# Kernel optimization log

Measured on AMD Instinct MI355X. Metric: run time of the kernel, lower is better.

The kernel has to match this reference:

```python
import jax, jax.numpy as jnp
import numpy as np

B, N, F, L, H, C = 128, 512, 128, 64, 128, 10

def setup_inputs() -> dict:
    key = jax.random.key(0)
    ks = jax.random.split(key, 20)
    s = 0.1
    return {
        "g": jax.random.uniform(ks[0], (B, N, N), dtype=jnp.float32) + 1e-3,
        "h": jax.random.normal(ks[1], (B, N, F), dtype=jnp.float32),
        "labels": jax.random.randint(ks[2], (B,), 0, C),
        "eps": jax.random.normal(ks[3], (B, N, 1), dtype=jnp.float32),
        "W_s": jax.random.normal(ks[4], (F, L), dtype=jnp.float32) * s,
        "b_s": jnp.zeros((L,), jnp.float32),
        "W_mu": jax.random.normal(ks[5], (L, 1), dtype=jnp.float32) * s,
        "b_mu": jnp.zeros((1,), jnp.float32),
        "W_lv": jax.random.normal(ks[6], (L, 1), dtype=jnp.float32) * s,
        "b_lv": jnp.zeros((1,), jnp.float32),
        "W_dec": jax.random.normal(ks[7], (1, L), dtype=jnp.float32) * s,
        "b_dec": jnp.zeros((L,), jnp.float32),
        "W1": jax.random.normal(ks[8], (L, H), dtype=jnp.float32) * s,
        "b1": jnp.zeros((H,), jnp.float32),
        "W2": jax.random.normal(ks[9], (H, C), dtype=jnp.float32) * s,
        "b2": jnp.zeros((C,), jnp.float32),
        "beta": jnp.array([50.0], jnp.float32),
    }

def _gcn(gn, x, W, b):
    # GCN layer: propagate then project then ELU activation (dropout = 0)
    return jax.nn.elu(jnp.einsum('bnm,bmf->bnf', gn, x) @ W + b)

def reference(g, h, labels, eps, W_s, b_s, W_mu, b_mu, W_lv, b_lv, W_dec, b_dec, W1, b1, W2, b2, beta):
    # norm_g: degrees = sum over dim 1; broadcast division normalizes COLUMNS
    # (torch g/degrees with degrees of shape [N] divides g[:, j] by degrees[j])
    deg = jnp.sum(g, axis=1)                      # [B, N]
    gn = g / deg[:, None, :]                      # column-normalized adjacency
    h1 = _gcn(gn, h, W_s, b_s)                    # [B, N, L]
    mu = _gcn(gn, h1, W_mu, b_mu)                 # [B, N, 1]
    lv = _gcn(gn, h1, W_lv, b_lv)                 # [B, N, 1]
    z = mu + eps * jnp.exp(0.5 * lv)              # reparameterize (training)
    v = jax.nn.sigmoid(beta[0] * z)               # [B, N, 1]
    d = _gcn(gn, v, W_dec, b_dec)                 # [B, N, L]
    hp = jnp.einsum('bnl,bn->bl', h1, v[..., 0])  # h.T @ v pooling -> [B, L]
    logits = jax.nn.log_softmax(jax.nn.elu(hp @ W1 + b1) @ W2 + b2, axis=1)
    nll = -jnp.mean(logits[jnp.arange(B), labels])
    mus = mu.reshape(-1, 1)
    lvs = lv.reshape(-1, 1)
    M = mus.shape[0]
    kl = (-0.5 / M) * jnp.mean(jnp.sum(1.0 + 2.0 * lvs - mus**2 - jnp.exp(lvs)**2, axis=1))
    mse = jnp.mean((h1 - d) ** 2)
    loss = nll + kl + mse
    acc = jnp.mean((jnp.argmax(logits, axis=1) == labels).astype(jnp.float32))
    return (loss, acc)
```

## Files before the change

### kernel.cpp

```cpp
#include <hip/hip_runtime.h>

#define B_  128
#define N_  512
#define F_  128
#define L_  64
#define H_  128
#define C_  10

typedef short  bf8_t  __attribute__((ext_vector_type(8)));
typedef float  f32x4  __attribute__((ext_vector_type(4)));
typedef unsigned short us8 __attribute__((ext_vector_type(8)));
typedef unsigned short us4 __attribute__((ext_vector_type(4)));

static __device__ __forceinline__ unsigned short f2bf(float x) {
    union { float f; unsigned u; } c; c.f = x;
    unsigned r = (c.u + 0x7fffu + ((c.u >> 16) & 1u)) >> 16;
    return (unsigned short)r;
}
static __device__ __forceinline__ float bf2f(unsigned short s) {
    union { unsigned u; float f; } c; c.u = ((unsigned)s) << 16;
    return c.f;
}
static __device__ __forceinline__ float elu(float x) { return x > 0.f ? x : expm1f(x); }

#define OFF_DEGP   0
#define OFF_DEG    524288
#define OFF_HPP    589824
#define OFF_KLP    655360
#define OFF_MSEP   655872
#define OFF_TMU    656896
#define OFF_TLV    722432
#define OFF_V      787968
#define OFF_W      853504
#define OFF_LP     919040
#define OFF_COR    919168
#define OFF_H1Q    919296
#define OFF_GBF    3016448
#define OFF_UBFT   19793664
#define OFF_WSTBF  21890816

__global__ __launch_bounds__(256) void k1_deg(const float* __restrict__ g,
                                              const float* __restrict__ Ws,
                                              float* __restrict__ deg_part,
                                              unsigned short* __restrict__ gbf,
                                              unsigned short* __restrict__ WsTbf) {
    const int c = blockIdx.x, b = blockIdx.y;
    if (c == 0 && b == 0) {
        for (int i = threadIdx.x; i < F_ * L_; i += 256) {
            int l = i >> 7, f = i & 127;
            WsTbf[i] = f2bf(Ws[f * L_ + l]);
        }
    }
    const int half = threadIdx.x >> 7, lane = threadIdx.x & 127;
    const int j  = lane * 4;
    const int i0 = c * 128 + half * 64;
    const float*    gp = g   + ((size_t)b * N_ + i0) * N_ + j;
    unsigned short* gq = gbf + ((size_t)b * N_ + i0) * N_ + j;
    float4 acc = make_float4(0.f, 0.f, 0.f, 0.f);
    #pragma unroll 8
    for (int r = 0; r < 64; ++r) {
        float4 v = *reinterpret_cast<const float4*>(gp + (size_t)r * N_);
        acc.x += v.x; acc.y += v.y; acc.z += v.z; acc.w += v.w;
        us4 q; q[0] = f2bf(v.x); q[1] = f2bf(v.y); q[2] = f2bf(v.z); q[3] = f2bf(v.w);
        *reinterpret_cast<us4*>(gq + (size_t)r * N_) = q;
    }
    *reinterpret_cast<float4*>(deg_part + (size_t)(b * 8 + c * 2 + half) * N_ + j) = acc;
}

__global__ __launch_bounds__(256) void k2_u(const float* __restrict__ h,
                                            const unsigned short* __restrict__ WsTbf,
                                            const float* __restrict__ deg_part,
                                            float* __restrict__ deg,
                                            unsigned short* __restrict__ ubfT) {
    __shared__ float tile[64 * 65];
    __shared__ float sdeg[64];
    const int b    = blockIdx.y;
    const int m0   = blockIdx.x * 64;
    const int tid  = threadIdx.x;
    const int wave = tid >> 6, lane = tid & 63;
    const int ml = lane & 15, q = lane >> 4;
    const int row0 = wave * 16;

    if (tid < 64) {
        int j = m0 + tid;
        float s = 0.f;
        #pragma unroll
        for (int k = 0; k < 8; ++k) s += deg_part[(size_t)(b * 8 + k) * N_ + j];
        sdeg[tid] = s;
        deg[b * N_ + j] = s;
    }

    const float* A = h + (size_t)(b * N_ + m0 + row0 + ml) * F_ + q * 8;
    const unsigned short* Bb = WsTbf + ml * F_ + q * 8;

    f32x4 acc[4] = {};
    #pragma unroll
    for (int kk = 0; kk < F_; kk += 32) {
        float4 a0 = *reinterpret_cast<const float4*>(A + kk);
        float4 a1 = *reinterpret_cast<const float4*>(A + kk + 4);
        union { unsigned short s[8]; bf8_t v; } av;
        av.s[0] = f2bf(a0.x); av.s[1] = f2bf(a0.y); av.s[2] = f2bf(a0.z); av.s[3] = f2bf(a0.w);
        av.s[4] = f2bf(a1.x); av.s[5] = f2bf(a1.y); av.s[6] = f2bf(a1.z); av.s[7] = f2bf(a1.w);
        #pragma unroll
        for (int i = 0; i < 4; ++i) {
            bf8_t bv = *reinterpret_cast<const bf8_t*>(Bb + i * 16 * F_ + kk);
            acc[i] = __builtin_amdgcn_mfma_f32_16x16x32_bf16(av.v, bv, acc[i], 0, 0, 0);
        }
    }
    __syncthreads();
    #pragma unroll
    for (int i = 0; i < 4; ++i) {
        int col = i * 16 + ml;
        #pragma unroll
        for (int r = 0; r < 4; ++r) {
            int rl = row0 + 4 * q + r;
            tile[rl * 65 + col] = acc[i][r] / sdeg[rl];
        }
    }
    __syncthreads();
    for (int jj = 0; jj < 16; ++jj) {
        int ll = wave + jj * 4;
        ubfT[(size_t)(b * L_ + ll) * N_ + m0 + lane] = f2bf(tile[lane * 65 + ll]);
    }
}

__global__ __launch_bounds__(256) void k3_h1(const unsigned short* __restrict__ gbf,
                                             const unsigned short* __restrict__ ubfT,
                                             const float* __restrict__ b_s,
                                             const float* __restrict__ Wmu,
                                             const float* __restrict__ Wlv,
                                             const float* __restrict__ deg,
                                             unsigned short* __restrict__ h1q,
                                             float* __restrict__ tmu, float* __restrict__ tlv) {
    const int b    = blockIdx.y;
    const int tid  = threadIdx.x;
    const int wave = tid >> 6, lane = tid & 63;
    const int row0 = blockIdx.x * 64 + wave * 16;
    const int ml = lane & 15, q = lane >> 4;

    const unsigned short* A  = gbf  + (size_t)(b * N_ + row0 + ml) * N_ + q * 8;
    const unsigned short* B0 = ubfT + (size_t)(b * L_ + ml) * N_ + q * 8;

    f32x4 acc[4] = {};
    #pragma unroll 2
    for (int k = 0; k < N_; k += 32) {
        bf8_t a = *reinterpret_cast<const bf8_t*>(A + k);
        #pragma unroll
        for (int i = 0; i < 4; ++i) {
            bf8_t bb = *reinterpret_cast<const bf8_t*>(B0 + (size_t)i * 16 * N_ + k);
            acc[i] = __builtin_amdgcn_mfma_f32_16x16x32_bf16(a, bb, acc[i], 0, 0, 0);
        }
    }
    float bsv[4], wm[4], wl[4];
    #pragma unroll
    for (int i = 0; i < 4; ++i) {
        int col = i * 16 + ml;
        bsv[i] = b_s[col]; wm[i] = Wmu[col]; wl[i] = Wlv[col];
    }
    #pragma unroll
    for (int r = 0; r < 4; ++r) {
        int row = row0 + 4 * q + r;
        float pm = 0.f, pl = 0.f;
        #pragma unroll
        for (int i = 0; i < 4; ++i) {
            float hv = elu(acc[i][r] + bsv[i]);
            h1q[(size_t)(b * N_ + row) * L_ + i * 16 + ml] = f2bf(hv);
            pm = fmaf(hv, wm[i], pm);
            pl = fmaf(hv, wl[i], pl);
        }
        #pragma unroll
        for (int o = 1; o < 16; o <<= 1) { pm += __shfl_xor(pm, o); pl += __shfl_xor(pl, o); }
        if (ml == 0) {
            float idg = 1.f / deg[b * N_ + row];
            tmu[b * N_ + row] = pm * idg;
            tlv[b * N_ + row] = pl * idg;
        }
    }
}

__global__ __launch_bounds__(256) void k5_v(const unsigned short* __restrict__ gbf,
                                            const float* __restrict__ tmu, const float* __restrict__ tlv,
                                            const float* __restrict__ eps, const float* __restrict__ deg,
                                            const float* __restrict__ bmu, const float* __restrict__ blv,
                                            const float* __restrict__ beta,
                                            float* __restrict__ v, float* __restrict__ w,
                                            float* __restrict__ kl_part) {
    __shared__ float kls[4];
    const int b = blockIdx.y;
    const int wave = threadIdx.x >> 6, lane = threadIdx.x & 63;
    const int n0 = (blockIdx.x * 4 + wave) * 32;

    const float* tmr = tmu + b * N_ + lane * 8;
    const float* tlr = tlv + b * N_ + lane * 8;
    float tm[8], tl[8];
    *reinterpret_cast<float4*>(tm)     = *reinterpret_cast<const float4*>(tmr);
    *reinterpret_cast<float4*>(tm + 4) = *reinterpret_cast<const float4*>(tmr + 4);
    *reinterpret_cast<float4*>(tl)     = *reinterpret_cast<const float4*>(tlr);
    *reinterpret_cast<float4*>(tl + 4) = *reinterpret_cast<const float4*>(tlr + 4);

    const unsigned short* gbase = gbf + (size_t)(b * N_ + n0) * N_ + lane * 8;
    float myamu = 0.f, myalv = 0.f;
    #pragma unroll 4
    for (int r = 0; r < 32; ++r) {
        us8 gv = *reinterpret_cast<const us8*>(gbase + (size_t)r * N_);
        float amu = 0.f, alv = 0.f;
        #pragma unroll
        for (int j = 0; j < 8; ++j) {
            float gf = bf2f(gv[j]);
            amu = fmaf(gf, tm[j], amu);
            alv = fmaf(gf, tl[j], alv);
        }
        #pragma unroll
        for (int o = 32; o; o >>= 1) { amu += __shfl_xor(amu, o); alv += __shfl_xor(alv, o); }
        if (lane == r) { myamu = amu; myalv = alv; }
    }
    float klv = 0.f;
    if (lane < 32) {
        int n = n0 + lane;
        float mu = elu(myamu + bmu[0]);
        float lv = elu(myalv + blv[0]);
        float z  = mu + eps[b * N_ + n] * expf(0.5f * lv);
        float vv = 1.f / (1.f + expf(-beta[0] * z));
        v[b * N_ + n] = vv;
        w[b * N_ + n] = vv / deg[b * N_ + n];
        float e = expf(lv);
        klv = 1.f + 2.f * lv - mu * mu - e * e;
    }
    #pragma unroll
    for (int o = 32; o; o >>= 1) klv += __shfl_xor(klv, o);
    if (lane == 0) kls[wave] = klv;
    __syncthreads();
    if (threadIdx.x == 0)
        kl_part[blockIdx.y * 4 + blockIdx.x] = kls[0] + kls[1] + kls[2] + kls[3];
}

__global__ __launch_bounds__(256) void k6_dec(const unsigned short* __restrict__ gbf,
                                              const float* __restrict__ w, const float* __restrict__ v,
                                              const unsigned short* __restrict__ h1q,
                                              const float* __restrict__ Wdec, const float* __restrict__ bdec,
                                              float* __restrict__ hp_part, float* __restrict__ mse_part) {
    __shared__ float hps[4 * 64];
    __shared__ float mses[4];
    const int b = blockIdx.y;
    const int n0 = blockIdx.x * 64;
    const int tid = threadIdx.x, wave = tid >> 6, lane = tid & 63;
    const float wd = Wdec[lane], bd = bdec[lane];

    const float* wrow = w + b * N_ + lane * 8;
    float wr[8];
    *reinterpret_cast<float4*>(wr)     = *reinterpret_cast<const float4*>(wrow);
    *reinterpret_cast<float4*>(wr + 4) = *reinterpret_cast<const float4*>(wrow + 4);

    const unsigned short* gbase = gbf + (size_t)(b * N_ + n0 + wave * 16) * N_ + lane * 8;
    float hpl = 0.f, msep = 0.f;
    #pragma unroll 2
    for (int t = 0; t < 16; ++t) {
        int n = n0 + wave * 16 + t;
        us8 gv = *reinterpret_cast<const us8*>(gbase + (size_t)t * N_);
        float p = 0.f;
        #pragma unroll
        for (int j = 0; j < 8; ++j) p = fmaf(bf2f(gv[j]), wr[j], p);
        #pragma unroll
        for (int o = 32; o; o >>= 1) p += __shfl_xor(p, o);
        float dv = elu(p * wd + bd);
        float h1v = bf2f(h1q[(size_t)(b * N_ + n) * L_ + lane]);
        float diff = h1v - dv;
        msep = fmaf(diff, diff, msep);
        hpl  = fmaf(h1v, v[b * N_ + n], hpl);
    }
    hps[wave * 64 + lane] = hpl;
    #pragma unroll
    for (int o = 32; o; o >>= 1) msep += __shfl_xor(msep, o);
    if (lane == 0) mses[wave] = msep;
    __syncthreads();
    if (tid < 64) {
        float s = hps[tid] + hps[64 + tid] + hps[128 + tid] + hps[192 + tid];
        hp_part[(size_t)blockIdx.x * (B_ * 64) + b * 64 + tid] = s;
    }
    if (tid == 0)
        mse_part[blockIdx.y * 8 + blockIdx.x] = mses[0] + mses[1] + mses[2] + mses[3];
}

__global__ __launch_bounds__(128) void k7a_head(const float* __restrict__ hp_part,
                                                const float* __restrict__ W1, const float* __restrict__ b1,
                                                const float* __restrict__ W2, const float* __restrict__ b2,
                                                const int* __restrict__ labels,
                                                float* __restrict__ lp, float* __restrict__ cor) {
    __shared__ float hps[64];
    __shared__ float acts[128];
    __shared__ float lgs[10];
    const int b = blockIdx.x, tid = threadIdx.x;
    if (tid < 64) {
        float s = 0.f;
        #pragma unroll
        for (int x = 0; x < 8; ++x) s += hp_part[(size_t)x * (B_ * 64) + b * 64 + tid];
        hps[tid] = s;
    }
    __syncthreads();
    float s0 = 0, s1 = 0, s2 = 0, s3 = 0;
    for (int l = 0; l < 64; l += 4) {
        s0 += hps[l]     * W1[(l)     * H_ + tid];
        s1 += hps[l + 1] * W1[(l + 1) * H_ + tid];
        s2 += hps[l + 2] * W1[(l + 2) * H_ + tid];
        s3 += hps[l + 3] * W1[(l + 3) * H_ + tid];
    }
    acts[tid] = elu((s0 + s1) + (s2 + s3) + b1[tid]);
    __syncthreads();
    if (tid < C_) {
        float lg = b2[tid];
        for (int hh = 0; hh < H_; ++hh) lg += acts[hh] * W2[hh * C_ + tid];
        lgs[tid] = lg;
    }
    __syncthreads();
    if (tid == 0) {
        float mx = lgs[0]; int am = 0;
        for (int c = 1; c < C_; ++c) if (lgs[c] > mx) { mx = lgs[c]; am = c; }
        float se = 0.f;
        for (int c = 0; c < C_; ++c) se += expf(lgs[c] - mx);
        int lbl = labels[b];
        lp[b]  = lgs[lbl] - mx - logf(se);
        cor[b] = (am == lbl) ? 1.f : 0.f;
    }
}

__global__ __launch_bounds__(128) void k7b_final(const float* __restrict__ lp, const float* __restrict__ cor,
                                                 const float* __restrict__ kl_part, const float* __restrict__ mse_part,
                                                 float* __restrict__ out) {
    __shared__ float r1[128], r2[128], r3[128], r4[128];
    int tid = threadIdx.x;
    r1[tid] = lp[tid]; r2[tid] = cor[tid];
    float k = 0.f, m = 0.f;
    #pragma unroll
    for (int i = 0; i < 4; ++i)  k += kl_part[tid + i * 128];
    #pragma unroll
    for (int i = 0; i < 8; ++i)  m += mse_part[tid + i * 128];
    r3[tid] = k; r4[tid] = m;
    __syncthreads();
    for (int o = 64; o; o >>= 1) {
        if (tid < o) { r1[tid] += r1[tid + o]; r2[tid] += r2[tid + o];
                       r3[tid] += r3[tid + o]; r4[tid] += r4[tid + o]; }
        __syncthreads();
    }
    if (tid == 0) {
        float nll = -r1[0] / (float)B_;
        float kl  = r3[0] * (-0.5f / (65536.f * 65536.f));
        float mse = r4[0] / (float)(B_ * N_ * L_);
        out[0] = nll + kl + mse;
        out[1] = r2[0] / (float)B_;
    }
}

extern "C" void kernel_launch(void* const* d_in, const int* in_sizes, int n_in,
                              void* d_out, int out_size, void* d_ws, size_t ws_size,
                              hipStream_t stream) {
    const float* g     = (const float*)d_in[0];
    const float* h     = (const float*)d_in[1];
    const int*   labels= (const int*)  d_in[2];
    const float* eps   = (const float*)d_in[3];
    const float* W_s   = (const float*)d_in[4];
    const float* b_s   = (const float*)d_in[5];
    const float* W_mu  = (const float*)d_in[6];
    const float* b_mu  = (const float*)d_in[7];
    const float* W_lv  = (const float*)d_in[8];
    const float* b_lv  = (const float*)d_in[9];
    const float* W_dec = (const float*)d_in[10];
    const float* b_dec = (const float*)d_in[11];
    const float* W1    = (const float*)d_in[12];
    const float* b1    = (const float*)d_in[13];
    const float* W2    = (const float*)d_in[14];
    const float* b2    = (const float*)d_in[15];
    const float* beta  = (const float*)d_in[16];

    float* ws = (float*)d_ws;
    float* deg_part = ws + OFF_DEGP;
    float* deg      = ws + OFF_DEG;
    float* hp_part  = ws + OFF_HPP;
    float* kl_part  = ws + OFF_KLP;
    float* mse_part = ws + OFF_MSEP;
    float* tmu      = ws + OFF_TMU;
    float* tlv      = ws + OFF_TLV;
    float* vv       = ws + OFF_V;
    float* wv       = ws + OFF_W;
    float* lp       = ws + OFF_LP;
    float* cor      = ws + OFF_COR;
    unsigned short* h1q   = (unsigned short*)(ws + OFF_H1Q);
    unsigned short* gbf   = (unsigned short*)(ws + OFF_GBF);
    unsigned short* ubfT  = (unsigned short*)(ws + OFF_UBFT);
    unsigned short* WsTbf = (unsigned short*)(ws + OFF_WSTBF);

    k1_deg  <<<dim3(4, B_), 256, 0, stream>>>(g, W_s, deg_part, gbf, WsTbf);
    k2_u    <<<dim3(8, B_), 256, 0, stream>>>(h, WsTbf, deg_part, deg, ubfT);
    k3_h1   <<<dim3(8, B_), 256, 0, stream>>>(gbf, ubfT, b_s, W_mu, W_lv, deg, h1q, tmu, tlv);
    k5_v    <<<dim3(4, B_), 256, 0, stream>>>(gbf, tmu, tlv, eps, deg, b_mu, b_lv, beta, vv, wv, kl_part);
    k6_dec  <<<dim3(8, B_), 256, 0, stream>>>(gbf, wv, vv, h1q, W_dec, b_dec, hp_part, mse_part);
    k7a_head<<<B_, 128, 0, stream>>>(hp_part, W1, b1, W2, b2, labels, lp, cor);
    k7b_final<<<1, 128, 0, stream>>>(lp, cor, kl_part, mse_part, (float*)d_out);
}
```

Baseline: 338.5 us.

## Fuse all per-graph stages into one 1024-thread block per batch element

Replaces the six per-stage kernels with a single kernel that gives each batch element one 1024-thread block. Degrees, v, w, the per-wave partial sums and a swizzled bf16 copy of W_s now live in shared memory, with block-level barriers between stages instead of kernel boundaries. This removes launch gaps and global round-trips for small intermediates. In exchange only 128 blocks run, which may underuse the GPU's compute units, and each block runs its phases serially.

```diff
diff --git a/kernel.cpp b/kernel.cpp
--- a/kernel.cpp
+++ b/kernel.cpp
@@ -10,7 +10,6 @@
 typedef short  bf8_t  __attribute__((ext_vector_type(8)));
 typedef float  f32x4  __attribute__((ext_vector_type(4)));
 typedef unsigned short us8 __attribute__((ext_vector_type(8)));
-typedef unsigned short us4 __attribute__((ext_vector_type(4)));
 
 static __device__ __forceinline__ unsigned short f2bf(float x) {
     union { float f; unsigned u; } c; c.f = x;
@@ -23,318 +22,290 @@
 }
 static __device__ __forceinline__ float elu(float x) { return x > 0.f ? x : expm1f(x); }
 
-#define OFF_DEGP   0
-#define OFF_DEG    524288
-#define OFF_HPP    589824
-#define OFF_KLP    655360
-#define OFF_MSEP   655872
-#define OFF_TMU    656896
-#define OFF_TLV    722432
-#define OFF_V      787968
-#define OFF_W      853504
-#define OFF_LP     919040
-#define OFF_COR    919168
-#define OFF_H1Q    919296
-#define OFF_GBF    3016448
-#define OFF_UBFT   19793664
-#define OFF_WSTBF  21890816
-
-__global__ __launch_bounds__(256) void k1_deg(const float* __restrict__ g,
-                                              const float* __restrict__ Ws,
-                                              float* __restrict__ deg_part,
-                                              unsigned short* __restrict__ gbf,
-                                              unsigned short* __restrict__ WsTbf) {
-    const int c = blockIdx.x, b = blockIdx.y;
-    if (c == 0 && b == 0) {
-        for (int i = threadIdx.x; i < F_ * L_; i += 256) {
+#define OFF_GBF   0
+#define OFF_UBFT  16777216
+#define OFF_H1Q   18874368
+#define OFF_KLP   20971520
+#define OFF_MSEP  20971648
+#define OFF_LP    20971776
+#define OFF_COR   20971904
+
+#define S_DEG   0
+#define S_TMU   512
+#define S_TLV   1024
+#define S_V     1536
+#define S_W     2048
+#define S_KL    2560
+#define S_MSE   2576
+#define S_LGS   2592
+#define S_HPS   2624
+#define S_HP    3648
+#define S_DEGP  512
+#define S_WST   8704
+#define S_TOT   12800
+
+__global__ __launch_bounds__(1024) void kmega(
+    const float* __restrict__ g, const float* __restrict__ h,
+    const int* __restrict__ labels, const float* __restrict__ eps,
+    const float* __restrict__ Ws, const float* __restrict__ b_s,
+    const float* __restrict__ Wmu, const float* __restrict__ bmu,
+    const float* __restrict__ Wlv, const float* __restrict__ blv,
+    const float* __restrict__ Wdec, const float* __restrict__ bdec,
+    const float* __restrict__ W1, const float* __restrict__ b1,
+    const float* __restrict__ W2, const float* __restrict__ b2,
+    const float* __restrict__ beta,
+    unsigned short* __restrict__ gbf, unsigned short* __restrict__ ubfT,
+    unsigned short* __restrict__ h1q,
+    float* __restrict__ klp, float* __restrict__ msep_g,
+    float* __restrict__ lp, float* __restrict__ cor)
+{
+    __shared__ float sm[S_TOT];
+    const int b   = blockIdx.x;
+    const int tid = threadIdx.x;
+    const int w   = tid >> 6, lane = tid & 63;
+    const int ml  = lane & 15, q = lane >> 4;
+
+    {
+        unsigned short* wst = (unsigned short*)(sm + S_WST);
+        for (int i = tid; i < F_ * L_; i += 1024) {
             int l = i >> 7, f = i & 127;
-            WsTbf[i] = f2bf(Ws[f * L_ + l]);
-        }
-    }
-    const int half = threadIdx.x >> 7, lane = threadIdx.x & 127;
-    const int j  = lane * 4;
-    const int i0 = c * 128 + half * 64;
-    const float*    gp = g   + ((size_t)b * N_ + i0) * N_ + j;
-    unsigned short* gq = gbf + ((size_t)b * N_ + i0) * N_ + j;
-    float4 acc = make_float4(0.f, 0.f, 0.f, 0.f);
-    #pragma unroll 8
-    for (int r = 0; r < 64; ++r) {
-        float4 v = *reinterpret_cast<const float4*>(gp + (size_t)r * N_);
-        acc.x += v.x; acc.y += v.y; acc.z += v.z; acc.w += v.w;
-        us4 q; q[0] = f2bf(v.x); q[1] = f2bf(v.y); q[2] = f2bf(v.z); q[3] = f2bf(v.w);
-        *reinterpret_cast<us4*>(gq + (size_t)r * N_) = q;
-    }
-    *reinterpret_cast<float4*>(deg_part + (size_t)(b * 8 + c * 2 + half) * N_ + j) = acc;
-}
-
-__global__ __launch_bounds__(256) void k2_u(const float* __restrict__ h,
-                                            const unsigned short* __restrict__ WsTbf,
-                                            const float* __restrict__ deg_part,
-                                            float* __restrict__ deg,
-                                            unsigned short* __restrict__ ubfT) {
-    __shared__ float tile[64 * 65];
-    __shared__ float sdeg[64];
-    const int b    = blockIdx.y;
-    const int m0   = blockIdx.x * 64;
-    const int tid  = threadIdx.x;
-    const int wave = tid >> 6, lane = tid & 63;
-    const int ml = lane & 15, q = lane >> 4;
-    const int row0 = wave * 16;
-
-    if (tid < 64) {
-        int j = m0 + tid;
+            wst[l * F_ + (f ^ ((l & 7) << 3))] = f2bf(Ws[f * L_ + l]);
+        }
+    }
+
+    {
+        const float*    gp = g   + ((size_t)b * N_ + w * 32) * N_ + lane * 8;
+        unsigned short* gq = gbf + ((size_t)b * N_ + w * 32) * N_ + lane * 8;
+        float cs[8] = {};
+        #pragma unroll 4
+        for (int r = 0; r < 32; ++r) {
+            float4 v0 = *reinterpret_cast<const float4*>(gp + (size_t)r * N_);
+            float4 v1 = *reinterpret_cast<const float4*>(gp + (size_t)r * N_ + 4);
+            cs[0] += v0.x; cs[1] += v0.y; cs[2] += v0.z; cs[3] += v0.w;
+            cs[4] += v1.x; cs[5] += v1.y; cs[6] += v1.z; cs[7] += v1.w;
+            us8 qv;
+            qv[0] = f2bf(v0.x); qv[1] = f2bf(v0.y); qv[2] = f2bf(v0.z); qv[3] = f2bf(v0.w);
+            qv[4] = f2bf(v1.x); qv[5] = f2bf(v1.y); qv[6] = f2bf(v1.z); qv[7] = f2bf(v1.w);
+            *reinterpret_cast<us8*>(gq + (size_t)r * N_) = qv;
+        }
+        #pragma unroll
+        for (int j = 0; j < 8; ++j) sm[S_DEGP + w * 512 + lane * 8 + j] = cs[j];
+    }
+    __syncthreads();
+    if (tid < 512) {
         float s = 0.f;
         #pragma unroll
-        for (int k = 0; k < 8; ++k) s += deg_part[(size_t)(b * 8 + k) * N_ + j];
-        sdeg[tid] = s;
-        deg[b * N_ + j] = s;
-    }
-
-    const float* A = h + (size_t)(b * N_ + m0 + row0 + ml) * F_ + q * 8;
-    const unsigned short* Bb = WsTbf + ml * F_ + q * 8;
-
-    f32x4 acc[4] = {};
-    #pragma unroll
-    for (int kk = 0; kk < F_; kk += 32) {
-        float4 a0 = *reinterpret_cast<const float4*>(A + kk);
-        float4 a1 = *reinterpret_cast<const float4*>(A + kk + 4);
-        union { unsigned short s[8]; bf8_t v; } av;
-        av.s[0] = f2bf(a0.x); av.s[1] = f2bf(a0.y); av.s[2] = f2bf(a0.z); av.s[3] = f2bf(a0.w);
-        av.s[4] = f2bf(a1.x); av.s[5] = f2bf(a1.y); av.s[6] = f2bf(a1.z); av.s[7] = f2bf(a1.w);
-        #pragma unroll
-        for (int i = 0; i < 4; ++i) {
-            bf8_t bv = *reinterpret_cast<const bf8_t*>(Bb + i * 16 * F_ + kk);
-            acc[i] = __builtin_amdgcn_mfma_f32_16x16x32_bf16(av.v, bv, acc[i], 0, 0, 0);
-        }
-    }
-    __syncthreads();
-    #pragma unroll
-    for (int i = 0; i < 4; ++i) {
-        int col = i * 16 + ml;
-        #pragma unroll
-        for (int r = 0; r < 4; ++r) {
-            int rl = row0 + 4 * q + r;
-            tile[rl * 65 + col] = acc[i][r] / sdeg[rl];
-        }
-    }
-    __syncthreads();
-    for (int jj = 0; jj < 16; ++jj) {
-        int ll = wave + jj * 4;
-        ubfT[(size_t)(b * L_ + ll) * N_ + m0 + lane] = f2bf(tile[lane * 65 + ll]);
-    }
-}
-
-__global__ __launch_bounds__(256) void k3_h1(const unsigned short* __restrict__ gbf,
-                                             const unsigned short* __restrict__ ubfT,
-                                             const float* __restrict__ b_s,
-                                             const float* __restrict__ Wmu,
-                                             const float* __restrict__ Wlv,
-                                             const float* __restrict__ deg,
-                                             unsigned short* __restrict__ h1q,
-                                             float* __restrict__ tmu, float* __restrict__ tlv) {
-    const int b    = blockIdx.y;
-    const int tid  = threadIdx.x;
-    const int wave = tid >> 6, lane = tid & 63;
-    const int row0 = blockIdx.x * 64 + wave * 16;
-    const int ml = lane & 15, q = lane >> 4;
-
-    const unsigned short* A  = gbf  + (size_t)(b * N_ + row0 + ml) * N_ + q * 8;
-    const unsigned short* B0 = ubfT + (size_t)(b * L_ + ml) * N_ + q * 8;
-
-    f32x4 acc[4] = {};
-    #pragma unroll 2
-    for (int k = 0; k < N_; k += 32) {
-        bf8_t a = *reinterpret_cast<const bf8_t*>(A + k);
-        #pragma unroll
-        for (int i = 0; i < 4; ++i) {
-            bf8_t bb = *reinterpret_cast<const bf8_t*>(B0 + (size_t)i * 16 * N_ + k);
-            acc[i] = __builtin_amdgcn_mfma_f32_16x16x32_bf16(a, bb, acc[i], 0, 0, 0);
-        }
-    }
-    float bsv[4], wm[4], wl[4];
-    #pragma unroll
-    for (int i = 0; i < 4; ++i) {
-        int col = i * 16 + ml;
-        bsv[i] = b_s[col]; wm[i] = Wmu[col]; wl[i] = Wlv[col];
-    }
-    #pragma unroll
-    for (int r = 0; r < 4; ++r) {
-        int row = row0 + 4 * q + r;
-        float pm = 0.f, pl = 0.f;
-        #pragma unroll
-        for (int i = 0; i < 4; ++i) {
-            float hv = elu(acc[i][r] + bsv[i]);
-            h1q[(size_t)(b * N_ + row) * L_ + i * 16 + ml] = f2bf(hv);
-            pm = fmaf(hv, wm[i], pm);
-            pl = fmaf(hv, wl[i], pl);
-        }
-        #pragma unroll
-        for (int o = 1; o < 16; o <<= 1) { pm += __shfl_xor(pm, o); pl += __shfl_xor(pl, o); }
-        if (ml == 0) {
-            float idg = 1.f / deg[b * N_ + row];
-            tmu[b * N_ + row] = pm * idg;
-            tlv[b * N_ + row] = pl * idg;
-        }
-    }
-}
-
-__global__ __launch_bounds__(256) void k5_v(const unsigned short* __restrict__ gbf,
-                                            const float* __restrict__ tmu, const float* __restrict__ tlv,
-                                            const float* __restrict__ eps, const float* __restrict__ deg,
-                                            const float* __restrict__ bmu, const float* __restrict__ blv,
-                                            const float* __restrict__ beta,
-                                            float* __restrict__ v, float* __restrict__ w,
-                                            float* __restrict__ kl_part) {
-    __shared__ float kls[4];
-    const int b = blockIdx.y;
-    const int wave = threadIdx.x >> 6, lane = threadIdx.x & 63;
-    const int n0 = (blockIdx.x * 4 + wave) * 32;
-
-    const float* tmr = tmu + b * N_ + lane * 8;
-    const float* tlr = tlv + b * N_ + lane * 8;
-    float tm[8], tl[8];
-    *reinterpret_cast<float4*>(tm)     = *reinterpret_cast<const float4*>(tmr);
-    *reinterpret_cast<float4*>(tm + 4) = *reinterpret_cast<const float4*>(tmr + 4);
-    *reinterpret_cast<float4*>(tl)     = *reinterpret_cast<const float4*>(tlr);
-    *reinterpret_cast<float4*>(tl + 4) = *reinterpret_cast<const float4*>(tlr + 4);
-
-    const unsigned short* gbase = gbf + (size_t)(b * N_ + n0) * N_ + lane * 8;
-    float myamu = 0.f, myalv = 0.f;
-    #pragma unroll 4
-    for (int r = 0; r < 32; ++r) {
-        us8 gv = *reinterpret_cast<const us8*>(gbase + (size_t)r * N_);
-        float amu = 0.f, alv = 0.f;
-        #pragma unroll
-        for (int j = 0; j < 8; ++j) {
-            float gf = bf2f(gv[j]);
-            amu = fmaf(gf, tm[j], amu);
-            alv = fmaf(gf, tl[j], alv);
-        }
-        #pragma unroll
-        for (int o = 32; o; o >>= 1) { amu += __shfl_xor(amu, o); alv += __shfl_xor(alv, o); }
-        if (lane == r) { myamu = amu; myalv = alv; }
-    }
-    float klv = 0.f;
-    if (lane < 32) {
-        int n = n0 + lane;
-        float mu = elu(myamu + bmu[0]);
-        float lv = elu(myalv + blv[0]);
-        float z  = mu + eps[b * N_ + n] * expf(0.5f * lv);
-        float vv = 1.f / (1.f + expf(-beta[0] * z));
-        v[b * N_ + n] = vv;
-        w[b * N_ + n] = vv / deg[b * N_ + n];
-        float e = expf(lv);
-        klv = 1.f + 2.f * lv - mu * mu - e * e;
-    }
-    #pragma unroll
-    for (int o = 32; o; o >>= 1) klv += __shfl_xor(klv, o);
-    if (lane == 0) kls[wave] = klv;
-    __syncthreads();
-    if (threadIdx.x == 0)
-        kl_part[blockIdx.y * 4 + blockIdx.x] = kls[0] + kls[1] + kls[2] + kls[3];
-}
-
-__global__ __launch_bounds__(256) void k6_dec(const unsigned short* __restrict__ gbf,
-                                              const float* __restrict__ w, const float* __restrict__ v,
-                                              const unsigned short* __restrict__ h1q,
-                                              const float* __restrict__ Wdec, const float* __restrict__ bdec,
-                                              float* __restrict__ hp_part, float* __restrict__ mse_part) {
-    __shared__ float hps[4 * 64];
-    __shared__ float mses[4];
-    const int b = blockIdx.y;
-    const int n0 = blockIdx.x * 64;
-    const int tid = threadIdx.x, wave = tid >> 6, lane = tid & 63;
-    const float wd = Wdec[lane], bd = bdec[lane];
-
-    const float* wrow = w + b * N_ + lane * 8;
-    float wr[8];
-    *reinterpret_cast<float4*>(wr)     = *reinterpret_cast<const float4*>(wrow);
-    *reinterpret_cast<float4*>(wr + 4) = *reinterpret_cast<const float4*>(wrow + 4);
-
-    const unsigned short* gbase = gbf + (size_t)(b * N_ + n0 + wave * 16) * N_ + lane * 8;
-    float hpl = 0.f, msep = 0.f;
-    #pragma unroll 2
-    for (int t = 0; t < 16; ++t) {
-        int n = n0 + wave * 16 + t;
-        us8 gv = *reinterpret_cast<const us8*>(gbase + (size_t)t * N_);
-        float p = 0.f;
-        #pragma unroll
-        for (int j = 0; j < 8; ++j) p = fmaf(bf2f(gv[j]), wr[j], p);
-        #pragma unroll
-        for (int o = 32; o; o >>= 1) p += __shfl_xor(p, o);
-        float dv = elu(p * wd + bd);
-        float h1v = bf2f(h1q[(size_t)(b * N_ + n) * L_ + lane]);
-        float diff = h1v - dv;
-        msep = fmaf(diff, diff, msep);
-        hpl  = fmaf(h1v, v[b * N_ + n], hpl);
-    }
-    hps[wave * 64 + lane] = hpl;
-    #pragma unroll
-    for (int o = 32; o; o >>= 1) msep += __shfl_xor(msep, o);
-    if (lane == 0) mses[wave] = msep;
-    __syncthreads();
-    if (tid < 64) {
-        float s = hps[tid] + hps[64 + tid] + hps[128 + tid] + hps[192 + tid];
-        hp_part[(size_t)blockIdx.x * (B_ * 64) + b * 64 + tid] = s;
-    }
-    if (tid == 0)
-        mse_part[blockIdx.y * 8 + blockIdx.x] = mses[0] + mses[1] + mses[2] + mses[3];
-}
-
-__global__ __launch_bounds__(128) void k7a_head(const float* __restrict__ hp_part,
-                                                const float* __restrict__ W1, const float* __restrict__ b1,
-                                                const float* __restrict__ W2, const float* __restrict__ b2,
-                                                const int* __restrict__ labels,
-                                                float* __restrict__ lp, float* __restrict__ cor) {
-    __shared__ float hps[64];
-    __shared__ float acts[128];
-    __shared__ float lgs[10];
-    const int b = blockIdx.x, tid = threadIdx.x;
+        for (int k = 0; k < 16; ++k) s += sm[S_DEGP + k * 512 + tid];
+        sm[S_DEG + tid] = s;
+    }
+    __syncthreads();
+
+    {
+        const unsigned short* wst = (const unsigned short*)(sm + S_WST);
+        #pragma unroll
+        for (int sub = 0; sub < 2; ++sub) {
+            const int m0 = (2 * w + sub) * 16;
+            const float* Bp = h + (size_t)(b * N_ + m0 + ml) * F_ + q * 8;
+            f32x4 acc[4] = {};
+            #pragma unroll
+            for (int kk = 0; kk < F_; kk += 32) {
+                float4 b0 = *reinterpret_cast<const float4*>(Bp + kk);
+                float4 b1 = *reinterpret_cast<const float4*>(Bp + kk + 4);
+                union { unsigned short s[8]; bf8_t v; } bv;
+                bv.s[0] = f2bf(b0.x); bv.s[1] = f2bf(b0.y); bv.s[2] = f2bf(b0.z); bv.s[3] = f2bf(b0.w);
+                bv.s[4] = f2bf(b1.x); bv.s[5] = f2bf(b1.y); bv.s[6] = f2bf(b1.z); bv.s[7] = f2bf(b1.w);
+                #pragma unroll
+                for (int i = 0; i < 4; ++i) {
+                    const int l = i * 16 + ml;
+                    bf8_t av = *reinterpret_cast<const bf8_t*>(
+                        wst + l * F_ + ((q * 8 + kk) ^ ((ml & 7) << 3)));
+                    acc[i] = __builtin_amdgcn_mfma_f32_16x16x32_bf16(av, bv.v, acc[i], 0, 0, 0);
+                }
+            }
+            const float idg = 1.f / sm[S_DEG + m0 + ml];
+            #pragma unroll
+            for (int i = 0; i < 4; ++i) {
+                #pragma unroll
+                for (int r = 0; r < 4; ++r) {
+                    int l = i * 16 + 4 * q + r;
+                    ubfT[(size_t)(b * L_ + l) * N_ + m0 + ml] = f2bf(acc[i][r] * idg);
+                }
+            }
+        }
+    }
+    __syncthreads();
+
+    {
+        #pragma unroll
+        for (int sub = 0; sub < 2; ++sub) {
+            const int row0 = w * 32 + sub * 16;
+            const unsigned short* A  = gbf  + (size_t)(b * N_ + row0 + ml) * N_ + q * 8;
+            const unsigned short* B0 = ubfT + (size_t)(b * L_ + ml) * N_ + q * 8;
+            f32x4 acc[4] = {};
+            #pragma unroll 4
+            for (int k = 0; k < N_; k += 32) {
+                bf8_t a = *reinterpret_cast<const bf8_t*>(A + k);
+                #pragma unroll
+                for (int i = 0; i < 4; ++i) {
+                    bf8_t bb = *reinterpret_cast<const bf8_t*>(B0 + (size_t)i * 16 * N_ + k);
+                    acc[i] = __builtin_amdgcn_mfma_f32_16x16x32_bf16(a, bb, acc[i], 0, 0, 0);
+                }
+            }
+            float bsv[4], wm[4], wl[4];
+            #pragma unroll
+            for (int i = 0; i < 4; ++i) {
+                int col = i * 16 + ml;
+                bsv[i] = b_s[col]; wm[i] = Wmu[col]; wl[i] = Wlv[col];
+            }
+            #pragma unroll
+            for (int r = 0; r < 4; ++r) {
+                int row = row0 + 4 * q + r;
+                float pm = 0.f, pl = 0.f;
+                #pragma unroll
+                for (int i = 0; i < 4; ++i) {
+                    float hv = elu(acc[i][r] + bsv[i]);
+                    h1q[(size_t)(b * N_ + row) * L_ + i * 16 + ml] = f2bf(hv);
+                    pm = fmaf(hv, wm[i], pm);
+                    pl = fmaf(hv, wl[i], pl);
+                }
+                #pragma unroll
+                for (int o = 1; o < 16; o <<= 1) { pm += __shfl_xor(pm, o); pl += __shfl_xor(pl, o); }
+                if (ml == 0) {
+                    float idg = 1.f / sm[S_DEG + row];
+                    sm[S_TMU + row] = pm * idg;
+                    sm[S_TLV + row] = pl * idg;
+                }
+            }
+        }
+    }
+    __syncthreads();
+
+    {
+        const int n0 = w * 32;
+        float tm[8], tl[8];
+        *reinterpret_cast<float4*>(tm)     = *reinterpret_cast<const float4*>(sm + S_TMU + lane * 8);
+        *reinterpret_cast<float4*>(tm + 4) = *reinterpret_cast<const float4*>(sm + S_TMU + lane * 8 + 4);
+        *reinterpret_cast<float4*>(tl)     = *reinterpret_cast<const float4*>(sm + S_TLV + lane * 8);
+        *reinterpret_cast<float4*>(tl + 4) = *reinterpret_cast<const float4*>(sm + S_TLV + lane * 8 + 4);
+
+        const unsigned short* gbase = gbf + (size_t)(b * N_ + n0) * N_ + lane * 8;
+        float myamu = 0.f, myalv = 0.f;
+        #pragma unroll 4
+        for (int r = 0; r < 32; ++r) {
+            us8 gv = *reinterpret_cast<const us8*>(gbase + (size_t)r * N_);
+            float amu = 0.f, alv = 0.f;
+            #pragma unroll
+            for (int j = 0; j < 8; ++j) {
+                float gf = bf2f(gv[j]);
+                amu = fmaf(gf, tm[j], amu);
+                alv = fmaf(gf, tl[j], alv);
+            }
+            #pragma unroll
+            for (int o = 32; o; o >>= 1) { amu += __shfl_xor(amu, o); alv += __shfl_xor(alv, o); }
+            if (lane == r) { myamu = amu; myalv = alv; }
+        }
+        float klv = 0.f;
+        if (lane < 32) {
+            int n = n0 + lane;
+            float mu = elu(myamu + bmu[0]);
+            float lv = elu(myalv + blv[0]);
+            float z  = mu + eps[b * N_ + n] * expf(0.5f * lv);
+            float vs = 1.f / (1.f + expf(-beta[0] * z));
+            sm[S_V + n] = vs;
+            sm[S_W + n] = vs / sm[S_DEG + n];
+            float e = expf(lv);
+            klv = 1.f + 2.f * lv - mu * mu - e * e;
+        }
+        #pragma unroll
+        for (int o = 32; o; o >>= 1) klv += __shfl_xor(klv, o);
+        if (lane == 0) sm[S_KL + w] = klv;
+    }
+    __syncthreads();
+
+    {
+        const int n0 = w * 32;
+        const float wd = Wdec[lane], bd = bdec[lane];
+        float wr[8];
+        *reinterpret_cast<float4*>(wr)     = *reinterpret_cast<const float4*>(sm + S_W + lane * 8);
+        *reinterpret_cast<float4*>(wr + 4) = *reinterpret_cast<const float4*>(sm + S_W + lane * 8 + 4);
+
+        const unsigned short* gbase = gbf + (size_t)(b * N_ + n0) * N_ + lane * 8;
+        float hpl = 0.f, msep = 0.f;
+        #pragma unroll 2
+        for (int t = 0; t < 32; ++t) {
+            int n = n0 + t;
+            us8 gv = *reinterpret_cast<const us8*>(gbase + (size_t)t * N_);
+            float p = 0.f;
+            #pragma unroll
+            for (int j = 0; j < 8; ++j) p = fmaf(bf2f(gv[j]), wr[j], p);
+            #pragma unroll
+            for (int o = 32; o; o >>= 1) p += __shfl_xor(p, o);
+            float dv  = elu(p * wd + bd);
+            float h1v = bf2f(h1q[(size_t)(b * N_ + n) * L_ + lane]);
+            float diff = h1v - dv;
+            msep = fmaf(diff, diff, msep);
+            hpl  = fmaf(h1v, sm[S_V + n], hpl);
+        }
+        sm[S_HPS + w * 64 + lane] = hpl;
+        #pragma unroll
+        for (int o = 32; o; o >>= 1) msep += __shfl_xor(msep, o);
+        if (lane == 0) sm[S_MSE + w] = msep;
+    }
+    __syncthreads();
+
     if (tid < 64) {
         float s = 0.f;
         #pragma unroll
-        for (int x = 0; x < 8; ++x) s += hp_part[(size_t)x * (B_ * 64) + b * 64 + tid];
-        hps[tid] = s;
-    }
-    __syncthreads();
-    float s0 = 0, s1 = 0, s2 = 0, s3 = 0;
-    for (int l = 0; l < 64; l += 4) {
-        s0 += hps[l]     * W1[(l)     * H_ + tid];
-        s1 += hps[l + 1] * W1[(l + 1) * H_ + tid];
-        s2 += hps[l + 2] * W1[(l + 2) * H_ + tid];
-        s3 += hps[l + 3] * W1[(l + 3) * H_ + tid];
-    }
-    acts[tid] = elu((s0 + s1) + (s2 + s3) + b1[tid]);
+        for (int k = 0; k < 16; ++k) s += sm[S_HPS + k * 64 + tid];
+        sm[S_HP + tid] = s;
+    }
+    __syncthreads();
+    if (tid < H_) {
+        float s0 = 0, s1 = 0, s2 = 0, s3 = 0;
+        for (int l = 0; l < 64; l += 4) {
+            s0 += sm[S_HP + l]     * W1[(l)     * H_ + tid];
+            s1 += sm[S_HP + l + 1] * W1[(l + 1) * H_ + tid];
+            s2 += sm[S_HP + l + 2] * W1[(l + 2) * H_ + tid];
+            s3 += sm[S_HP + l + 3] * W1[(l + 3) * H_ + tid];
+        }
+        sm[S_TLV + tid] = elu((s0 + s1) + (s2 + s3) + b1[tid]);
+    }
     __syncthreads();
     if (tid < C_) {
         float lg = b2[tid];
-        for (int hh = 0; hh < H_; ++hh) lg += acts[hh] * W2[hh * C_ + tid];
-        lgs[tid] = lg;
+        for (int hh = 0; hh < H_; ++hh) lg += sm[S_TLV + hh] * W2[hh * C_ + tid];
+        sm[S_LGS + tid] = lg;
     }
     __syncthreads();
     if (tid == 0) {
-        float mx = lgs[0]; int am = 0;
-        for (int c = 1; c < C_; ++c) if (lgs[c] > mx) { mx = lgs[c]; am = c; }
+        float mx = sm[S_LGS]; int am = 0;
+        for (int c = 1; c < C_; ++c) if (sm[S_LGS + c] > mx) { mx = sm[S_LGS + c]; am = c; }
         float se = 0.f;
-        for (int c = 0; c < C_; ++c) se += expf(lgs[c] - mx);
+        for (int c = 0; c < C_; ++c) se += expf(sm[S_LGS + c] - mx);
         int lbl = labels[b];
-        lp[b]  = lgs[lbl] - mx - logf(se);
+        lp[b]  = sm[S_LGS + lbl] - mx - logf(se);
         cor[b] = (am == lbl) ? 1.f : 0.f;
     }
+    if (tid == 64) {
+        float kk = 0.f;
+        #pragma unroll
+        for (int i = 0; i < 16; ++i) kk += sm[S_KL + i];
+        klp[b] = kk;
+    }
+    if (tid == 65) {
+        float mm = 0.f;
+        #pragma unroll
+        for (int i = 0; i < 16; ++i) mm += sm[S_MSE + i];
+        msep_g[b] = mm;
+    }
 }
 
 __global__ __launch_bounds__(128) void k7b_final(const float* __restrict__ lp, const float* __restrict__ cor,
-                                                 const float* __restrict__ kl_part, const float* __restrict__ mse_part,
+                                                 const float* __restrict__ klp, const float* __restrict__ msep,
                                                  float* __restrict__ out) {
     __shared__ float r1[128], r2[128], r3[128], r4[128];
     int tid = threadIdx.x;
-    r1[tid] = lp[tid]; r2[tid] = cor[tid];
-    float k = 0.f, m = 0.f;
-    #pragma unroll
-    for (int i = 0; i < 4; ++i)  k += kl_part[tid + i * 128];
-    #pragma unroll
-    for (int i = 0; i < 8; ++i)  m += mse_part[tid + i * 128];
-    r3[tid] = k; r4[tid] = m;
+    r1[tid] = lp[tid]; r2[tid] = cor[tid]; r3[tid] = klp[tid]; r4[tid] = msep[tid];
     __syncthreads();
     for (int o = 64; o; o >>= 1) {
         if (tid < o) { r1[tid] += r1[tid + o]; r2[tid] += r2[tid + o];
@@ -357,14 +328,14 @@
     const float* h     = (const float*)d_in[1];
     const int*   labels= (const int*)  d_in[2];
     const float* eps   = (const float*)d_in[3];
-    const float* W_s   = (const float*)d_in[4];
+    const float* Ws    = (const float*)d_in[4];
     const float* b_s   = (const float*)d_in[5];
-    const float* W_mu  = (const float*)d_in[6];
-    const float* b_mu  = (const float*)d_in[7];
-    const float* W_lv  = (const float*)d_in[8];
-    const float* b_lv  = (const float*)d_in[9];
-    const float* W_dec = (const float*)d_in[10];
-    const float* b_dec = (const float*)d_in[11];
+    const float* Wmu   = (const float*)d_in[6];
+    const float* bmu   = (const float*)d_in[7];
+    const float* Wlv   = (const float*)d_in[8];
+    const float* blv   = (const float*)d_in[9];
+    const float* Wdec  = (const float*)d_in[10];
+    const float* bdec  = (const float*)d_in[11];
     const float* W1    = (const float*)d_in[12];
     const float* b1    = (const float*)d_in[13];
     const float* W2    = (const float*)d_in[14];
@@ -372,27 +343,16 @@
     const float* beta  = (const float*)d_in[16];
 
     float* ws = (float*)d_ws;
-    float* deg_part = ws + OFF_DEGP;
-    float* deg      = ws + OFF_DEG;
-    float* hp_part  = ws + OFF_HPP;
-    float* kl_part  = ws + OFF_KLP;
-    float* mse_part = ws + OFF_MSEP;
-    float* tmu      = ws + OFF_TMU;
-    float* tlv      = ws + OFF_TLV;
-    float* vv       = ws + OFF_V;
-    float* wv       = ws + OFF_W;
-    float* lp       = ws + OFF_LP;
-    float* cor      = ws + OFF_COR;
-    unsigned short* h1q   = (unsigned short*)(ws + OFF_H1Q);
-    unsigned short* gbf   = (unsigned short*)(ws + OFF_GBF);
-    unsigned short* ubfT  = (unsigned short*)(ws + OFF_UBFT);
-    unsigned short* WsTbf = (unsigned short*)(ws + OFF_WSTBF);
-
-    k1_deg  <<<dim3(4, B_), 256, 0, stream>>>(g, W_s, deg_part, gbf, WsTbf);
-    k2_u    <<<dim3(8, B_), 256, 0, stream>>>(h, WsTbf, deg_part, deg, ubfT);
-    k3_h1   <<<dim3(8, B_), 256, 0, stream>>>(gbf, ubfT, b_s, W_mu, W_lv, deg, h1q, tmu, tlv);
-    k5_v    <<<dim3(4, B_), 256, 0, stream>>>(gbf, tmu, tlv, eps, deg, b_mu, b_lv, beta, vv, wv, kl_part);
-    k6_dec  <<<dim3(8, B_), 256, 0, stream>>>(gbf, wv, vv, h1q, W_dec, b_dec, hp_part, mse_part);
-    k7a_head<<<B_, 128, 0, stream>>>(hp_part, W1, b1, W2, b2, labels, lp, cor);
-    k7b_final<<<1, 128, 0, stream>>>(lp, cor, kl_part, mse_part, (float*)d_out);
-}
+    unsigned short* gbf  = (unsigned short*)(ws + OFF_GBF);
+    unsigned short* ubfT = (unsigned short*)(ws + OFF_UBFT);
+    unsigned short* h1q  = (unsigned short*)(ws + OFF_H1Q);
+    float* klp  = ws + OFF_KLP;
+    float* msep = ws + OFF_MSEP;
+    float* lp   = ws + OFF_LP;
+    float* cor  = ws + OFF_COR;
+
+    kmega<<<B_, 1024, 0, stream>>>(g, h, labels, eps, Ws, b_s, Wmu, bmu, Wlv, blv,
+                                   Wdec, bdec, W1, b1, W2, b2, beta,
+                                   gbf, ubfT, h1q, klp, msep, lp, cor);
+    k7b_final<<<1, 128, 0, stream>>>(lp, cor, klp, msep, (float*)d_out);
+}
```

After: 381.1 us. +12.6%, slower.
